# Optimization experiments

Hardware: AMD Instinct MI355X
Metric: run time of the kernel (lower is better)

Reference implementation:

```python
import jax, jax.numpy as jnp
import numpy as np

C = 8; E = 512; HEADS = 8; DH = E // HEADS; M = 256; PINV_ITERS = 6; KW = 33

def layer_norm(x, g, b):
    mu = x.mean(-1, keepdims=True)
    xm = x - mu
    v = (xm * xm).mean(-1, keepdims=True)
    return xm / jnp.sqrt(v + 1e-5) * g + b

def mp_pinv(x, iters=PINV_ITERS):
    # Moore-Penrose pseudoinverse via Newton-Schulz iterations (lucidrains nystrom-attention)
    I = jnp.eye(x.shape[-1], dtype=x.dtype)
    ax = jnp.abs(x)
    z = jnp.swapaxes(x, -1, -2) / (jnp.max(ax.sum(-2)) * jnp.max(ax.sum(-1)))
    for _ in range(iters):
        xz = x @ z
        z = 0.25 * z @ (13. * I - xz @ (15. * I - xz @ (7. * I - xz)))
    return z

def nystrom_attn(x, mask, Wqkv, Wout, bout, conv_w):
    b, n0, d = x.shape
    pad = (-n0) % M  # left-pad so seq divisible by num_landmarks
    x = jnp.pad(x, ((0, 0), (pad, 0), (0, 0)))
    mask = jnp.pad(mask, ((0, 0), (pad, 0)))
    n = n0 + pad
    qkv = (x @ Wqkv).reshape(b, n, 3, HEADS, DH).transpose(2, 0, 3, 1, 4)
    q, k, v = qkv[0], qkv[1], qkv[2]  # [b,h,n,dh]
    mf = mask[:, None, :, None].astype(x.dtype)
    q = q * mf * (DH ** -0.5); k = k * mf; v = v * mf
    l = n // M
    mls = mask.reshape(b, 1, M, l).sum(-1).astype(x.dtype)  # valid count per landmark segment
    div = mls[..., None] + 1e-8
    ql = q.reshape(b, HEADS, M, l, DH).sum(3) / div
    kl = k.reshape(b, HEADS, M, l, DH).sum(3) / div
    mland = mls > 0  # [b,1,M]
    neg = -jnp.finfo(x.dtype).max / 2
    sim1 = jnp.where(mask[:, None, :, None] & mland[..., None, :], jnp.einsum('bhid,bhjd->bhij', q, kl), neg)
    sim2 = jnp.where(mland[..., :, None] & mland[..., None, :], jnp.einsum('bhid,bhjd->bhij', ql, kl), neg)
    sim3 = jnp.where(mland[..., :, None] & mask[:, None, None, :], jnp.einsum('bhid,bhjd->bhij', ql, k), neg)
    a1 = jax.nn.softmax(sim1, -1); a2 = jax.nn.softmax(sim2, -1); a3 = jax.nn.softmax(sim3, -1)
    out = (a1 @ mp_pinv(a2)) @ (a3 @ v)
    # residual depthwise conv over sequence dim (residual=True in NystromAttention)
    out = out + jax.lax.conv_general_dilated(v, conv_w, (1, 1), ((KW // 2, KW // 2), (0, 0)),
                                             dimension_numbers=('NCHW', 'OIHW', 'NCHW'),
                                             feature_group_count=HEADS)
    out = out.transpose(0, 2, 1, 3).reshape(b, n, d) @ Wout + bout
    return out[:, pad:]

def _forward(h, W1, b1, cls_token, pmt_token, ln1_g, ln1_b, Wqkv1, Wout1, bout1, conv1,
             ln0_g, ln0_b, Wqkv0, Wout0, bout0, conv0, lnf_g, lnf_b, W3, b3):
    N = h.shape[0]
    h1 = jax.nn.relu(h @ W1 + b1)  # _fc1
    seq = jnp.concatenate([cls_token, pmt_token, h1], 0)[None]  # [1, 1+C+N, E]
    y = nystrom_attn(layer_norm(seq, ln1_g, ln1_b), jnp.ones((1, seq.shape[1]), bool),
                     Wqkv1, Wout1, bout1, conv1)
    x = seq + y  # layer1 (TransLayer_custom)
    pmt = x[:, 1:1 + C, :]   # new pmt tokens [1,C,E]
    toks = x[:, 1 + C:, :]   # [1,N,E]
    assn = jax.nn.softmax(jnp.einsum('bnd,bcd->bnc', toks, pmt), -1)
    idx = jnp.argmax(assn[0], -1)  # [N] cluster assignment
    # cluster dispatch: per-cluster [pmt_i; tokens-of-cluster-i] run of shared layer0, via masking
    xs = jnp.concatenate([pmt[0][:, None, :], jnp.broadcast_to(toks[0], (C, N, E))], 1)  # [C,1+N,E]
    masks = jnp.concatenate([jnp.ones((C, 1), bool), idx[None, :] == jnp.arange(C)[:, None]], 1)
    def trans0(xi, mi):
        xi = xi[None]
        return (xi + nystrom_attn(layer_norm(xi, ln0_g, ln0_b), mi[None], Wqkv0, Wout0, bout0, conv0))[0]
    out = jax.vmap(trans0)(xs, masks)  # [C,1+N,E]
    h_un = out[:, 1:, :][idx, jnp.arange(N)]  # each token from its own cluster's run
    order = jnp.argsort(idx)  # stable: groups tokens by cluster, preserving order (concat order)
    h_global = h_un[order]; idx_new = idx[order]
    hcat = jnp.concatenate([x[0, 0][None], h_global], 0)  # [1+N, E]
    hn = layer_norm(hcat, lnf_g, lnf_b)
    sums = jax.ops.segment_sum(hcat[1:], idx_new, num_segments=C)
    counts = jax.ops.segment_sum(jnp.ones((N,), h.dtype), idx_new, num_segments=C)
    merge = sums / jnp.maximum(counts, 1.)[:, None]  # CTM merge token per cluster
    ptc = jnp.linalg.norm(pmt[0] @ pmt[0].T - jnp.eye(C, dtype=h.dtype))
    tok_out = jnp.concatenate([hn[0][None], merge], 0).mean(0)
    logit = tok_out @ W3 + b3
    return logit, ptc

def setup_inputs() -> dict:
    key = jax.random.key(0)
    ks = jax.random.split(key, 16)
    N, IN_DIM, NC = 4096, 1024, 2
    s = 0.02
    q, _ = jnp.linalg.qr(jax.random.normal(ks[15], (E, C)))  # orthonormal pmt init
    return {
        'h': jax.random.normal(ks[0], (N, IN_DIM)),
        'W1': jax.random.normal(ks[1], (IN_DIM, E)) * s, 'b1': jnp.zeros((E,)),
        'cls_token': jax.random.normal(ks[2], (1, E)),
        'pmt_token': q.T,
        'ln1_g': jnp.ones((E,)), 'ln1_b': jnp.zeros((E,)),
        'Wqkv1': jax.random.normal(ks[3], (E, 3 * E)) * s,
        'Wout1': jax.random.normal(ks[4], (E, E)) * s, 'bout1': jnp.zeros((E,)),
        'conv1': jax.random.normal(ks[5], (HEADS, 1, KW, 1)) * s,
        'ln0_g': jnp.ones((E,)), 'ln0_b': jnp.zeros((E,)),
        'Wqkv0': jax.random.normal(ks[6], (E, 3 * E)) * s,
        'Wout0': jax.random.normal(ks[7], (E, E)) * s, 'bout0': jnp.zeros((E,)),
        'conv0': jax.random.normal(ks[8], (HEADS, 1, KW, 1)) * s,
        'lnf_g': jnp.ones((E,)), 'lnf_b': jnp.zeros((E,)),
        'W3': jax.random.normal(ks[9], (E, NC)) * s, 'b3': jnp.zeros((NC,)),
    }

def reference(h, W1, b1, cls_token, pmt_token, ln1_g, ln1_b, Wqkv1, Wout1, bout1, conv1,
              ln0_g, ln0_b, Wqkv0, Wout0, bout0, conv0, lnf_g, lnf_b, W3, b3):
    logit, ptc = _forward(h, W1, b1, cls_token, pmt_token, ln1_g, ln1_b, Wqkv1, Wout1, bout1, conv1,
                          ln0_g, ln0_b, Wqkv0, Wout0, bout0, conv0, lnf_g, lnf_b, W3, b3)
    return (logit[None], jax.nn.softmax(logit)[None], ptc)
```

## Files before the change

### kernel.cpp

```cpp
#include <hip/hip_runtime.h>

#define NEGV (-1.70141173e38f)

constexpr int E    = 512;
constexpr int NTOK = 4096;
constexpr int NPAD = 4352;
constexpr int PAD1 = 247;
constexpr int NSEQ = 4105;
constexpr int NG   = 5120;
constexpr int NTP  = 4104;

typedef __attribute__((ext_vector_type(8))) short short8;
typedef __attribute__((ext_vector_type(4))) float float4v;

__device__ inline float bf2f(ushort u){ return __uint_as_float(((unsigned)u)<<16); }
__device__ inline ushort f2bf(float f){
  unsigned u = __float_as_uint(f);
  unsigned r = (u + 0x7FFFu + ((u>>16)&1u)) >> 16;
  return (ushort)r;
}
__device__ inline uint4 packu4(const ushort* u) {
  uint4 w;
  w.x = (unsigned)u[0] | ((unsigned)u[1] << 16);
  w.y = (unsigned)u[2] | ((unsigned)u[3] << 16);
  w.z = (unsigned)u[4] | ((unsigned)u[5] << 16);
  w.w = (unsigned)u[6] | ((unsigned)u[7] << 16);
  return w;
}

template<int BT, bool BOUNDS>
__global__ __launch_bounds__(256) void k_mm(
    const ushort* __restrict__ A, const ushort* __restrict__ B,
    const float* __restrict__ bias, const float* __restrict__ resid,
    float* __restrict__ Cf, ushort* __restrict__ Cb,
    int M, int N, int K, int ksplit, int ldC,
    long sA, long sB, long sC,
    const int* __restrict__ colsel, const int* __restrict__ rowsel,
    int zmodA, int zmodB, const int* __restrict__ krange, int kshift,
    float alpha, float bdiag, int flags)
{
  const int z = blockIdx.z;
  const int batch = z / ksplit, ks = z - batch * ksplit;
  const int kslice = K / ksplit;
  int kbeg = ks * kslice, kend = kbeg + kslice;
  if (krange) { int ki = batch >> kshift; kbeg = krange[2*ki]; kend = krange[2*ki+1]; }
  long aoff;
  if (colsel) { int s = colsel[blockIdx.x]; if (s < 0) s = 0; aoff = (long)(s*8 + batch) * sA; }
  else aoff = (long)(zmodA ? (batch & (zmodA-1)) : batch) * sA;
  long boff;
  if (rowsel) { int s = rowsel[blockIdx.y]; if (s < 0) s = 0; boff = (long)(s*8 + batch) * sB; }
  else boff = (long)(zmodB ? (batch & (zmodB-1)) : batch) * sB;
  A += aoff; B += boff;
  const long coff = (long)z * sC;

  __shared__ __align__(16) ushort Al[4][128][8];
  __shared__ __align__(16) ushort Bl[4][128][8];

  const int tid  = threadIdx.x;
  const int lane = tid & 63, wid = tid >> 6;
  const int wr = wid >> 1, wc = wid & 1;
  const int l4 = lane >> 4, l15 = lane & 15;
  const int row0 = blockIdx.y * 128, col0 = blockIdx.x * 128;

  float4v acc[4][4];
#pragma unroll
  for (int i = 0; i < 4; ++i)
#pragma unroll
    for (int j = 0; j < 4; ++j) acc[i][j] = (float4v){0.f,0.f,0.f,0.f};

  for (int k0 = kbeg; k0 < kend; k0 += 32) {
    __syncthreads();
#pragma unroll
    for (int e = 0; e < 2; ++e) {
      int id = tid * 2 + e; int m = id >> 2, kb = id & 3;
      uint4 v = make_uint4(0u,0u,0u,0u);
      int gr = row0 + m;
      if (!BOUNDS || gr < M)
        v = *reinterpret_cast<const uint4*>(A + (long)gr * K + k0 + kb * 8);
      *reinterpret_cast<uint4*>(&Al[kb][m][0]) = v;
    }
    if (BT) {
#pragma unroll
      for (int e = 0; e < 2; ++e) {
        int id = tid * 2 + e; int n = id >> 2, kb = id & 3;
        uint4 v = make_uint4(0u,0u,0u,0u);
        int gc = col0 + n;
        if (!BOUNDS || gc < N)
          v = *reinterpret_cast<const uint4*>(B + (long)gc * K + k0 + kb * 8);
        *reinterpret_cast<uint4*>(&Bl[kb][n][0]) = v;
      }
    } else {
      int n = tid & 127, gc = col0 + n;
      bool inb = (!BOUNDS || gc < N);
#pragma unroll
      for (int e = 0; e < 2; ++e) {
        int kb = (tid >> 7) * 2 + e;
        ushort u[8];
#pragma unroll
        for (int j = 0; j < 8; ++j) {
          int gk = k0 + kb * 8 + j;
          ushort val = inb ? B[(long)gk * N + gc] : (ushort)0;
          if (flags & 4) {
            float f = bdiag * (gk == gc ? 1.f : 0.f) - bf2f(val);
            val = f2bf(f);
          }
          u[j] = val;
        }
        *reinterpret_cast<uint4*>(&Bl[kb][n][0]) = packu4(u);
      }
    }
    __syncthreads();
    short8 af[4], bg[4];
#pragma unroll
    for (int mi = 0; mi < 4; ++mi)
      af[mi] = *reinterpret_cast<const short8*>(&Al[l4][wr*64 + mi*16 + l15][0]);
#pragma unroll
    for (int ni = 0; ni < 4; ++ni)
      bg[ni] = *reinterpret_cast<const short8*>(&Bl[l4][wc*64 + ni*16 + l15][0]);
#pragma unroll
    for (int mi = 0; mi < 4; ++mi)
#pragma unroll
      for (int ni = 0; ni < 4; ++ni)
        acc[mi][ni] = __builtin_amdgcn_mfma_f32_16x16x32_bf16(af[mi], bg[ni], acc[mi][ni], 0, 0, 0);
  }
#pragma unroll
  for (int mi = 0; mi < 4; ++mi)
#pragma unroll
    for (int ni = 0; ni < 4; ++ni)
#pragma unroll
      for (int r = 0; r < 4; ++r) {
        int row = row0 + wr*64 + mi*16 + l4*4 + r;
        int col = col0 + wc*64 + ni*16 + l15;
        if (BOUNDS && (row >= M || col >= N)) continue;
        float v = alpha * acc[mi][ni][r];
        if (flags & 1) v += bias[col];
        if (flags & 2) v = fmaxf(v, 0.f);
        if (flags & 8) v += resid[(long)row * ldC + col];
        long off = coff + (long)row * ldC + col;
        if (flags & 16) Cb[off] = f2bf(v); else Cf[off] = v;
      }
}

static void mm(hipStream_t st, const void* A, const void* B, const float* bias, const float* resid,
               float* Cf, ushort* Cb, int M, int N, int K, int nb, int ksplit, int ldC,
               long sA, long sB, long sC,
               const int* colsel, const int* rowsel, int zmodA, int zmodB,
               const int* krange, int kshift,
               float alpha, float bdiag, int flags, bool bt, bool bounds)
{
  dim3 g((N + 127) / 128, (M + 127) / 128, nb * ksplit), b(256);
  const ushort* a = (const ushort*)A; const ushort* bb = (const ushort*)B;
  if (bt) {
    if (bounds) k_mm<1, true ><<<g, b, 0, st>>>(a, bb, bias, resid, Cf, Cb, M, N, K, ksplit, ldC, sA, sB, sC, colsel, rowsel, zmodA, zmodB, krange, kshift, alpha, bdiag, flags);
    else        k_mm<1, false><<<g, b, 0, st>>>(a, bb, bias, resid, Cf, Cb, M, N, K, ksplit, ldC, sA, sB, sC, colsel, rowsel, zmodA, zmodB, krange, kshift, alpha, bdiag, flags);
  } else {
    if (bounds) k_mm<0, true ><<<g, b, 0, st>>>(a, bb, bias, resid, Cf, Cb, M, N, K, ksplit, ldC, sA, sB, sC, colsel, rowsel, zmodA, zmodB, krange, kshift, alpha, bdiag, flags);
    else        k_mm<0, false><<<g, b, 0, st>>>(a, bb, bias, resid, Cf, Cb, M, N, K, ksplit, ldC, sA, sB, sC, colsel, rowsel, zmodA, zmodB, krange, kshift, alpha, bdiag, flags);
  }
}

__global__ __launch_bounds__(256, 1) void k_pinv(
    const ushort* __restrict__ X,
    ushort* __restrict__ ZA, ushort* __restrict__ ZAt,
    ushort* __restrict__ ZB, ushort* __restrict__ ZBt,
    ushort* __restrict__ Y,  ushort* __restrict__ Yt,
    ushort* __restrict__ T1, ushort* __restrict__ T1t,
    ushort* __restrict__ T2, ushort* __restrict__ T2t,
    float* __restrict__ sc, int nb, int* __restrict__ bars)
{
  __shared__ __align__(16) ushort SH[8448];
  ushort* AlF = SH;
  ushort* BlF = SH + 4096;
  const int tid = threadIdx.x;
  const int nblk = gridDim.x;
  int bi = 0;

  auto BAR = [&]() {
    __syncthreads();
    if (tid == 0) {
      __threadfence();
      atomicAdd(&bars[bi], 1);
      while (atomicAdd(&bars[bi], 0) < nblk) __builtin_amdgcn_s_sleep(2);
    }
    ++bi;
    __syncthreads();
    __threadfence();
  };

  {
    int ncl = nb >> 3;
    if ((int)blockIdx.x < ncl) {
      float* red = (float*)SH;
      int cl = blockIdx.x;
      float cmax = 0.f;
      for (int h = 0; h < 8; ++h) {
        const ushort* mat = X + (long)(cl * 8 + h) * 65536;
        float cs = 0.f;
        for (int i = 0; i < 256; ++i) cs += bf2f(mat[i * 256 + tid]);
        cmax = fmaxf(cmax, cs);
      }
      red[tid] = cmax; __syncthreads();
      for (int o = 128; o > 0; o >>= 1) { if (tid < o) red[tid] = fmaxf(red[tid], red[tid+o]); __syncthreads(); }
      if (tid == 0) sc[cl] = 1.f / red[0];
    }
    BAR();
  }

  const int ntile = nb * 4;

  {
    ushort (*lds2)[264] = (ushort(*)[264])SH;
    for (int tile = blockIdx.x; tile < ntile; tile += nblk) {
      int bt = tile >> 2, q = tile & 3;
      int row0 = (q >> 1) * 128, col0 = (q & 1) * 128;
      float scale = sc[bt >> 3];
      const ushort* Xb = X + (long)bt * 65536;
      ushort* Z0  = ZA  + (long)bt * 65536;
      ushort* Z0t = ZAt + (long)bt * 65536;
#pragma unroll
      for (int e = 0; e < 8; ++e) {
        int id = tid + e * 256;
        int r = id >> 4, ch = (id & 15) * 8;
        const ushort* src = Xb + (long)(row0 + r) * 256 + col0 + ch;
        ushort u[8];
#pragma unroll
        for (int j = 0; j < 8; ++j) u[j] = f2bf(bf2f(src[j]) * scale);
        *reinterpret_cast<uint4*>(Z0t + (long)(row0 + r) * 256 + col0 + ch) = packu4(u);
      }
      for (int s = 0; s < 4; ++s) {
        __syncthreads();
#pragma unroll
        for (int e = 0; e < 2; ++e) {
          int id = tid * 2 + e;
          int sr = id >> 4, ch = (id & 15) * 8;
          *reinterpret_cast<uint4*>(&lds2[sr][ch]) =
            *reinterpret_cast<const uint4*>(Xb + (long)(col0 + s * 32 + sr) * 256 + row0 + ch);
        }
        __syncthreads();
#pragma unroll
        for (int e = 0; e < 2; ++e) {
          int id = tid * 2 + e;
          int orow = id >> 2, oseg = (id & 3) * 8;
          ushort u[8];
#pragma unroll
          for (int j = 0; j < 8; ++j) u[j] = f2bf(bf2f(lds2[oseg + j][orow]) * scale);
          *reinterpret_cast<uint4*>(Z0 + (long)(row0 + orow) * 256 + col0 + s * 32 + oseg) = packu4(u);
        }
      }
      __syncthreads();
    }
    BAR();
  }

  const int lane = tid & 63, wid = tid >> 6;
  const int wr = wid >> 1, wc = wid & 1;
  const int l4 = lane >> 4, l15 = lane & 15;

  auto GEMM = [&](const ushort* A, const ushort* Bt, ushort* C, ushort* Ct,
                  float alpha, float bdiag, bool diag) {
    for (int tile = blockIdx.x; tile < ntile; tile += nblk) {
      int bt = tile >> 2, q = tile & 3;
      int row0 = (q >> 1) * 128, col0 = (q & 1) * 128;
      const ushort* Ab = A + (long)bt * 65536;
      const ushort* Bb = Bt + (long)bt * 65536;
      float4v acc[4][4];
#pragma unroll
      for (int i = 0; i < 4; ++i)
#pragma unroll
        for (int j = 0; j < 4; ++j) acc[i][j] = (float4v){0.f,0.f,0.f,0.f};
      for (int k0 = 0; k0 < 256; k0 += 32) {
        __syncthreads();
#pragma unroll
        for (int e = 0; e < 2; ++e) {
          int id = tid * 2 + e; int m = id >> 2, kb = id & 3;
          *reinterpret_cast<uint4*>(AlF + kb * 1024 + m * 8) =
            *reinterpret_cast<const uint4*>(Ab + (long)(row0 + m) * 256 + k0 + kb * 8);
        }
#pragma unroll
        for (int e = 0; e < 2; ++e) {
          int id = tid * 2 + e; int n = id >> 2, kb = id & 3;
          uint4 v = *reinterpret_cast<const uint4*>(Bb + (long)(col0 + n) * 256 + k0 + kb * 8);
          if (diag) {
            const ushort* up = reinterpret_cast<const ushort*>(&v);
            ushort u2[8];
#pragma unroll
            for (int j = 0; j < 8; ++j) {
              int gk = k0 + kb * 8 + j;
              u2[j] = f2bf(bdiag * (gk == (col0 + n) ? 1.f : 0.f) - bf2f(up[j]));
            }
            v = packu4(u2);
          }
          *reinterpret_cast<uint4*>(BlF + kb * 1024 + n * 8) = v;
        }
        __syncthreads();
        short8 af[4], bg[4];
#pragma unroll
        for (int mi = 0; mi < 4; ++mi)
          af[mi] = *reinterpret_cast<const short8*>(AlF + l4 * 1024 + (wr * 64 + mi * 16 + l15) * 8);
#pragma unroll
        for (int ni = 0; ni < 4; ++ni)
          bg[ni] = *reinterpret_cast<const short8*>(BlF + l4 * 1024 + (wc * 64 + ni * 16 + l15) * 8);
#pragma unroll
        for (int mi = 0; mi < 4; ++mi)
#pragma unroll
          for (int ni = 0; ni < 4; ++ni)
            acc[mi][ni] = __builtin_amdgcn_mfma_f32_16x16x32_bf16(af[mi], bg[ni], acc[mi][ni], 0, 0, 0);
      }
      long cb = (long)bt * 65536;
#pragma unroll
      for (int mi = 0; mi < 4; ++mi)
#pragma unroll
        for (int ni = 0; ni < 4; ++ni)
#pragma unroll
          for (int r = 0; r < 4; ++r) {
            int row = row0 + wr * 64 + mi * 16 + l4 * 4 + r;
            int col = col0 + wc * 64 + ni * 16 + l15;
            ushort val = f2bf(alpha * acc[mi][ni][r]);
            C[cb + (long)row * 256 + col] = val;
            Ct[cb + (long)col * 256 + row] = val;
          }
      __syncthreads();
    }
  };

  for (int it = 0; it < 6; ++it) {
    ushort* Zc  = (it & 1) ? ZB  : ZA;
    ushort* Zct = (it & 1) ? ZBt : ZAt;
    ushort* Zn  = (it & 1) ? ZA  : ZB;
    ushort* Znt = (it & 1) ? ZAt : ZBt;
    GEMM(X,  Zct, Y,  Yt,  1.f,    0.f, false); BAR();
    GEMM(Y,  Yt,  T1, T1t, 1.f,    7.f, true);  BAR();
    GEMM(Y,  T1t, T2, T2t, 1.f,   15.f, true);  BAR();
    GEMM(Zc, T2t, Zn, Znt, 0.25f, 13.f, true);
    if (it < 5) BAR();
  }
}

__global__ void k_prep0(const float* __restrict__ cls, const float* __restrict__ pmt, float* __restrict__ seq) {
  int i = blockIdx.x * 256 + threadIdx.x;
  if (i < 512) seq[i] = cls[i];
  else if (i < 4608) seq[i] = pmt[i - 512];
}
__global__ void k_cvt(const float* __restrict__ s, ushort* __restrict__ d, long n) {
  long i = (long)blockIdx.x * 256 + threadIdx.x;
  if (i < n) d[i] = f2bf(s[i]);
}
__global__ void k_tcvt_all(const float* __restrict__ W1, const float* __restrict__ Wq1,
                           const float* __restrict__ Wq0, const float* __restrict__ Wo1,
                           const float* __restrict__ Wo0,
                           ushort* __restrict__ W1t, ushort* __restrict__ Wq1t,
                           ushort* __restrict__ Wq0t, ushort* __restrict__ Wo1t,
                           ushort* __restrict__ Wo0t) {
  const float* W; ushort* Wt; int K, N;
  switch (blockIdx.z) {
    case 0:  W = W1;  Wt = W1t;  K = 1024; N = 512;  break;
    case 1:  W = Wq1; Wt = Wq1t; K = 512;  N = 1536; break;
    case 2:  W = Wq0; Wt = Wq0t; K = 512;  N = 1536; break;
    case 3:  W = Wo1; Wt = Wo1t; K = 512;  N = 512;  break;
    default: W = Wo0; Wt = Wo0t; K = 512;  N = 512;  break;
  }
  int nb_ = blockIdx.x * 32, kb = blockIdx.y * 32;
  if (nb_ >= N || kb >= K) return;
  __shared__ float tile[32][33];
  int tx = threadIdx.x, ty = threadIdx.y;
  for (int r = ty; r < 32; r += 8) tile[r][tx] = W[(long)(kb + r) * N + nb_ + tx];
  __syncthreads();
  for (int r = ty; r < 32; r += 8) Wt[(long)(nb_ + r) * K + kb + tx] = f2bf(tile[tx][r]);
}

__device__ __forceinline__ void ln_row(const float* __restrict__ xr, const float* __restrict__ g,
                                       const float* __restrict__ b, ushort* __restrict__ yr,
                                       float* red, int t) {
  float v0 = xr[t], v1 = xr[t + 256];
  red[t] = v0 + v1; __syncthreads();
  for (int o = 128; o > 0; o >>= 1) { if (t < o) red[t] += red[t + o]; __syncthreads(); }
  float mu = red[0] * (1.f / E); __syncthreads();
  float d0 = v0 - mu, d1 = v1 - mu;
  red[t] = d0 * d0 + d1 * d1; __syncthreads();
  for (int o = 128; o > 0; o >>= 1) { if (t < o) red[t] += red[t + o]; __syncthreads(); }
  float inv = 1.f / sqrtf(red[0] * (1.f / E) + 1e-5f);
  yr[t]       = f2bf(d0 * inv * g[t]       + b[t]);
  yr[t + 256] = f2bf(d1 * inv * g[t + 256] + b[t + 256]);
}

__global__ __launch_bounds__(256) void k_lnB(const float* __restrict__ x, const float* __restrict__ g,
                                             const float* __restrict__ b, ushort* __restrict__ y) {
  int row = blockIdx.x, t = threadIdx.x;
  ushort* yr = y + (long)row * E;
  if (row < PAD1) { yr[t] = 0; yr[t + 256] = 0; return; }
  __shared__ float red[256];
  ln_row(x + (long)(row - PAD1) * E, g, b, yr, red, t);
}
__global__ __launch_bounds__(256) void k_lnC(const float* __restrict__ seq, const float* __restrict__ g,
                                             const float* __restrict__ b, ushort* __restrict__ y) {
  int row = blockIdx.x, t = threadIdx.x;
  const float* xr = (row < 8) ? (seq + 512 + (long)row * E) : (seq + 9 * 512 + (long)(row - 8) * E);
  __shared__ float red[256];
  ln_row(xr, g, b, y + (long)row * E, red, t);
}

__global__ void k_buildQKVB(const float* __restrict__ qkv, ushort* __restrict__ Qb,
                            ushort* __restrict__ Kb, ushort* __restrict__ Vt) {
  int h = blockIdx.y, p0 = blockIdx.x * 64;
  int tx = threadIdx.x & 63, tg = threadIdx.x >> 6;
  __shared__ float tile[64][65];
  for (int r = tg; r < 64; r += 4) {
    long src = (long)(p0 + r) * 1536 + h * 64 + tx;
    long o = ((long)h * NPAD + p0 + r) * 64 + tx;
    Qb[o] = f2bf(qkv[src]);
    Kb[o] = f2bf(qkv[src + 512]);
    tile[r][tx] = qkv[src + 1024];
  }
  __syncthreads();
  for (int d = tg; d < 64; d += 4) Vt[((long)h * 64 + d) * NPAD + p0 + tx] = f2bf(tile[tx][d]);
}
__global__ void k_gatherQKV(const float* __restrict__ qkvall, const int* __restrict__ gtok,
                            ushort* __restrict__ Qg, ushort* __restrict__ Kg, ushort* __restrict__ Vgt) {
  int h = blockIdx.y, p0 = blockIdx.x * 64;
  int tx = threadIdx.x & 63, tg = threadIdx.x >> 6;
  __shared__ float tile[64][65];
  for (int r = tg; r < 64; r += 4) {
    int tk = gtok[p0 + r];
    int srcrow = tk >= 0 ? 8 + tk : (tk <= -2 ? (-2 - tk) : -1);
    float q = 0.f, k = 0.f, v = 0.f;
    if (srcrow >= 0) {
      long s = (long)srcrow * 1536 + h * 64 + tx;
      q = qkvall[s]; k = qkvall[s + 512]; v = qkvall[s + 1024];
    }
    long o = ((long)h * NG + p0 + r) * 64 + tx;
    Qg[o] = f2bf(q); Kg[o] = f2bf(k);
    tile[r][tx] = v;
  }
  __syncthreads();
  for (int d = tg; d < 64; d += 4) Vgt[((long)h * 64 + d) * NG + p0 + tx] = f2bf(tile[tx][d]);
}

__global__ void k_qlkl_B(const float* __restrict__ qkv, ushort* __restrict__ ql, ushort* __restrict__ kl,
                         float* __restrict__ mlandB) {
  int i = blockIdx.x, h = blockIdx.y, d = threadIdx.x;
  float sq = 0.f, sk = 0.f; int cnt = 0;
  for (int j = 0; j < 17; ++j) {
    int p = i * 17 + j;
    if (p >= PAD1) {
      sq += qkv[(long)p * 1536 + h * 64 + d];
      sk += qkv[(long)p * 1536 + 512 + h * 64 + d];
      cnt++;
    }
  }
  float dv = (float)cnt + 1e-8f;
  ql[((long)h * 256 + i) * 64 + d] = f2bf(sq * 0.125f / dv);
  kl[((long)h * 256 + i) * 64 + d] = f2bf(sk / dv);
  if (h == 0 && d == 0) mlandB[i] = cnt > 0 ? 1.f : 0.f;
}

__global__ void k_qlkl_C(const float* __restrict__ qkvall, const int* __restrict__ idx,
                         ushort* __restrict__ qlc, ushort* __restrict__ klc,
                         float* __restrict__ mland_c) {
  int i = blockIdx.x, bt = blockIdx.y;
  int c = bt >> 3, h = bt & 7, d = threadIdx.x;
  float sq = 0.f, sk = 0.f; int cnt = 0;
  for (int j = 0; j < 17; ++j) {
    int p = i * 17 + j;
    int srcrow = -1;
    if (p == 255) srcrow = c;
    else if (p >= 256 && idx[p - 256] == c) srcrow = 8 + (p - 256);
    if (srcrow >= 0) {
      const float* src = qkvall + (long)srcrow * 1536 + h * 64;
      sq += src[d]; sk += src[512 + d];
      cnt++;
    }
  }
  float dv = (float)cnt + 1e-8f;
  qlc[((long)bt * 256 + i) * 64 + d] = f2bf(sq * 0.125f / dv);
  klc[((long)bt * 256 + i) * 64 + d] = f2bf(sk / dv);
  if (h == 0 && d == 0) mland_c[c * 256 + i] = cnt > 0 ? 1.f : 0.f;
}

__global__ __launch_bounds__(256) void k_a2soft(const float* __restrict__ S2, const float* __restrict__ mland,
                                                ushort* __restrict__ X) {
  int i = blockIdx.x, bt = blockIdx.y, j = threadIdx.x;
  int cl = bt >> 3;
  const float* Sr = S2 + ((long)bt * 256 + i) * 256;
  __shared__ float red[256];
  float landi = mland[cl * 256 + i];
  float out;
  if (landi > 0.f) {
    bool valid = mland[cl * 256 + j] > 0.f;
// ... 182 lines not shown
  }
  if (t == 0) {
    int s = 0;
    for (int c = 0; c < 8; ++c) {
      segs[c] = s;
      base[c] = s + 1;
      int tt2 = 1 + tot[c];
      krange[2 * c] = s;
      krange[2 * c + 1] = s + ((tt2 + 31) & ~31);
      s += (tt2 + 127) & ~127;
    }
    segs[8] = s;
    for (int c = 0; c <= 8; ++c) segb[c] = segs[c];
  }
  __syncthreads();
  for (int g = t; g < NG; g += 256) { gtok[g] = -1; gclu[g] = -1; }
  __syncthreads();
  if (t < 8) { gtok[segs[t]] = -2 - t; gclu[segs[t]] = t; }
  for (int b = t; b < NG / 128; b += 256) {
    int cl = -1;
    for (int c = 0; c < 8; ++c) if (b * 128 >= segs[c] && b * 128 < segs[c + 1]) cl = c;
    blkclu[b] = cl;
  }
  for (int b = 0; b < 16; ++b) {
    int c = myc[b];
    int rankw = 0;
    for (int cc = 0; cc < 8; ++cc) {
      unsigned long long m = __ballot(c == cc);
      if (c == cc) rankw = __popcll(m & ltmask);
      if (lane == 0) wcnt[w][cc] = __popcll(m);
    }
    __syncthreads();
    int off = base[c] + rankw;
    for (int w2 = 0; w2 < w; ++w2) off += wcnt[w2][c];
    int n = b * 256 + t;
    gtok[off] = n; gclu[off] = c; gpos[n] = off;
    __syncthreads();
    if (t < 8) base[t] += wcnt[0][t] + wcnt[1][t] + wcnt[2][t] + wcnt[3][t];
    __syncthreads();
  }
}

__global__ void k_outC(const float* __restrict__ OUTg, const int* __restrict__ gpos,
                       const int* __restrict__ idx, const float* __restrict__ qkvall,
                       const float* __restrict__ w, ushort* __restrict__ lnb) {
  int n = blockIdx.x, t = threadIdx.x;
  int h = t >> 6;
  int c = idx[n];
  float acc = OUTg[(long)gpos[n] * 512 + t];
  for (int tt = 0; tt < 33; ++tt) {
    int m = n + tt - 16;
    float vv = 0.f;
    if (m == -1) vv = qkvall[(long)c * 1536 + 1024 + t];
    else if (m >= 0 && m < NTOK && idx[m] == c) vv = qkvall[(long)(8 + m) * 1536 + 1024 + t];
    acc += vv * w[h * 33 + tt];
  }
  lnb[(long)n * E + t] = f2bf(acc);
}

__global__ void k_seg_part(const float* __restrict__ hun, const int* __restrict__ idx,
                           float* __restrict__ part, float* __restrict__ pcnt) {
  int c = blockIdx.x, sl = blockIdx.y, d = threadIdx.x;
  float s = 0.f; int cnt = 0;
  for (int n = sl * 256; n < sl * 256 + 256; ++n) {
    if (idx[n] == c) { s += hun[(long)n * E + d]; if (d == 0) cnt++; }
  }
  part[(long)(c * 16 + sl) * E + d] = s;
  if (d == 0) pcnt[c * 16 + sl] = (float)cnt;
}

__global__ void k_final(const float* __restrict__ x0, const float* __restrict__ g, const float* __restrict__ b,
                        const float* __restrict__ part, const float* __restrict__ pcnt,
                        const float* __restrict__ ptc, const float* __restrict__ W3, const float* __restrict__ b3,
                        float* __restrict__ out) {
  int t = threadIdx.x;
  __shared__ float red[512];
  float xv = x0[t];
  red[t] = xv; __syncthreads();
  for (int o = 256; o > 0; o >>= 1) { if (t < o) red[t] += red[t + o]; __syncthreads(); }
  float mu = red[0] * (1.f / 512.f); __syncthreads();
  float d0 = xv - mu;
  red[t] = d0 * d0; __syncthreads();
  for (int o = 256; o > 0; o >>= 1) { if (t < o) red[t] += red[t + o]; __syncthreads(); }
  float inv = 1.f / sqrtf(red[0] * (1.f / 512.f) + 1e-5f);
  __syncthreads();
  float acc = d0 * inv * g[t] + b[t];
  for (int c = 0; c < 8; ++c) {
    float s = 0.f, cnt = 0.f;
    for (int sl = 0; sl < 16; ++sl) { s += part[(long)(c * 16 + sl) * E + t]; cnt += pcnt[c * 16 + sl]; }
    acc += s / fmaxf(cnt, 1.f);
  }
  float tk = acc * (1.f / 9.f);
  red[t] = tk * W3[t * 2 + 0]; __syncthreads();
  for (int o = 256; o > 0; o >>= 1) { if (t < o) red[t] += red[t + o]; __syncthreads(); }
  float l0 = red[0] + b3[0]; __syncthreads();
  red[t] = tk * W3[t * 2 + 1]; __syncthreads();
  for (int o = 256; o > 0; o >>= 1) { if (t < o) red[t] += red[t + o]; __syncthreads(); }
  float l1 = red[0] + b3[1];
  if (t == 0) {
    out[0] = l0; out[1] = l1;
    float mx = fmaxf(l0, l1);
    float e0 = expf(l0 - mx), e1 = expf(l1 - mx), s = e0 + e1;
    out[2] = e0 / s; out[3] = e1 / s;
    out[4] = *ptc;
  }
}

extern "C" void kernel_launch(void* const* d_in, const int* in_sizes, int n_in,
                              void* d_out, int out_size, void* d_ws, size_t ws_size,
                              hipStream_t stream) {
  const float* h_in  = (const float*)d_in[0];
  const float* W1    = (const float*)d_in[1];
  const float* b1    = (const float*)d_in[2];
  const float* cls   = (const float*)d_in[3];
  const float* pmt_t = (const float*)d_in[4];
  const float* ln1_g = (const float*)d_in[5];
  const float* ln1_b = (const float*)d_in[6];
  const float* Wqkv1 = (const float*)d_in[7];
  const float* Wout1 = (const float*)d_in[8];
  const float* bout1 = (const float*)d_in[9];
  const float* conv1 = (const float*)d_in[10];
  const float* ln0_g = (const float*)d_in[11];
  const float* ln0_b = (const float*)d_in[12];
  const float* Wqkv0 = (const float*)d_in[13];
  const float* Wout0 = (const float*)d_in[14];
  const float* bout0 = (const float*)d_in[15];
  const float* conv0 = (const float*)d_in[16];
  const float* lnf_g = (const float*)d_in[17];
  const float* lnf_b = (const float*)d_in[18];
  const float* W3    = (const float*)d_in[19];
  const float* b3    = (const float*)d_in[20];

  char* base = (char*)d_ws;
  size_t off = 0;
  auto alloc = [&](size_t b) -> void* {
    off = (off + 255) & ~(size_t)255;
    void* p = base + off; off += b; return p;
  };
  float*  SEQ    = (float*) alloc((size_t)NSEQ * E * 4);
  float*  QKV    = (float*) alloc((size_t)NPAD * 1536 * 4);
  ushort* W1t    = (ushort*)alloc((size_t)512 * 1024 * 2);
  ushort* Wq1t   = (ushort*)alloc((size_t)1536 * 512 * 2);
  ushort* Wq0t   = (ushort*)alloc((size_t)1536 * 512 * 2);
  ushort* Wo1t   = (ushort*)alloc((size_t)512 * 512 * 2);
  ushort* Wo0t   = (ushort*)alloc((size_t)512 * 512 * 2);
  ushort* LNb    = (ushort*)alloc((size_t)NPAD * E * 2);
  ushort* QbU    = (ushort*)alloc((size_t)8 * NG * 64 * 2);
  ushort* KbU    = (ushort*)alloc((size_t)8 * NG * 64 * 2);
  ushort* VtU    = (ushort*)alloc((size_t)8 * NG * 64 * 2);
  char*   U1     = (char*)  alloc((size_t)8 * 256 * NG * 4);
  char*   U2     = (char*)  alloc((size_t)8 * 256 * NG * 2);
  ushort* PXb    = (ushort*)alloc((size_t)64 * 65536 * 2);
  ushort* PZa    = (ushort*)alloc((size_t)64 * 65536 * 2);
  ushort* PZat   = (ushort*)alloc((size_t)64 * 65536 * 2);
  ushort* qlbB   = (ushort*)alloc((size_t)8 * 16384 * 2);
  ushort* klbB   = (ushort*)alloc((size_t)8 * 16384 * 2);
  ushort* qlcb   = (ushort*)alloc((size_t)64 * 16384 * 2);
  ushort* klcb   = (ushort*)alloc((size_t)64 * 16384 * 2);
  float*  avsl   = (float*) alloc((size_t)8 * 8 * 16384 * 4);
  ushort* avb    = (ushort*)alloc((size_t)64 * 16384 * 2);
  ushort* Wcb    = (ushort*)alloc((size_t)64 * 16384 * 2);
  float*  PREOUT = (float*) alloc((size_t)NPAD * E * 4);
  float*  mlandB = (float*) alloc(256 * 4);
  float*  mlandC = (float*) alloc(8 * 256 * 4);
  int*    idx    = (int*)   alloc(NTOK * 4);
  int*    gtok   = (int*)   alloc(NG * 4);
  int*    gclu   = (int*)   alloc(NG * 4);
  int*    gpos   = (int*)   alloc(NTOK * 4);
  int*    segb   = (int*)   alloc(9 * 4);
  int*    krange = (int*)   alloc(16 * 4);
  int*    blkclu = (int*)   alloc((NG / 128) * 4);
  float*  ptc    = (float*) alloc(256);
  float*  sc     = (float*) alloc(256);
  int*    bars   = (int*)   alloc(64 * 4);
  float*  part   = (float*) alloc((size_t)8 * 16 * 512 * 4);
  float*  pcnt   = (float*) alloc(8 * 16 * 4);

  ushort* hb   = (ushort*)U1;
  float*  Sbuf = (float*)U1;
  ushort* Yp   = (ushort*)U1;
  ushort* Ytp  = (ushort*)(U1 + 1L * 8388608);
  ushort* T1p  = (ushort*)(U1 + 2L * 8388608);
  ushort* T1tp = (ushort*)(U1 + 3L * 8388608);
  ushort* T2p  = (ushort*)(U1 + 4L * 8388608);
  float*  OUTg = (float*)U1;
  ushort* Pbuf = (ushort*)U2;
  ushort* ZBp  = (ushort*)U2;
  ushort* ZBtp = (ushort*)U2 + 4194304;
  ushort* T2tp = (ushort*)avsl;

  hipMemsetAsync(bars, 0, 64 * sizeof(int), stream);

  k_tcvt_all<<<dim3(48, 32, 5), dim3(32, 8), 0, stream>>>(W1, Wqkv1, Wqkv0, Wout1, Wout0,
                                                          W1t, Wq1t, Wq0t, Wo1t, Wo0t);
  k_prep0<<<dim3(18), dim3(256), 0, stream>>>(cls, pmt_t, SEQ);
  k_cvt<<<dim3(16384), dim3(256), 0, stream>>>(h_in, hb, (long)4096 * 1024);
  mm(stream, hb, W1t, b1, nullptr, SEQ + 9 * 512, nullptr, 4096, 512, 1024, 1, 1, 512,
     0, 0, 0, nullptr, nullptr, 0, 0, nullptr, 0, 1.f, 0.f, 1 | 2, true, false);

  k_lnB<<<dim3(NPAD), dim3(256), 0, stream>>>(SEQ, ln1_g, ln1_b, LNb);
  mm(stream, LNb, Wq1t, nullptr, nullptr, QKV, nullptr, NPAD, 1536, 512, 1, 1, 1536,
     0, 0, 0, nullptr, nullptr, 0, 0, nullptr, 0, 1.f, 0.f, 0, true, false);
  k_buildQKVB<<<dim3(NPAD / 64, 8), dim3(256), 0, stream>>>(QKV, QbU, KbU, VtU);
  k_qlkl_B<<<dim3(256, 8), dim3(64), 0, stream>>>(QKV, qlbB, klbB, mlandB);
  mm(stream, qlbB, klbB, nullptr, nullptr, Sbuf, nullptr, 256, 256, 64, 8, 1, 256,
     16384, 16384, 65536, nullptr, nullptr, 0, 0, nullptr, 0, 1.f, 0.f, 0, true, false);
  k_a2soft<<<dim3(256, 8), dim3(256), 0, stream>>>(Sbuf, mlandB, PXb);
  k_pinv<<<dim3(256), dim3(256), 0, stream>>>(PXb, PZa, PZat, ZBp, ZBtp, Yp, Ytp, T1p, T1tp, T2p, T2tp,
                                              sc, 8, bars);
  mm(stream, qlbB, KbU, nullptr, nullptr, Sbuf, nullptr, 256, NPAD, 64, 8, 1, NPAD,
     16384, (long)NPAD * 64, (long)256 * NPAD, nullptr, nullptr, 0, 0, nullptr, 0, 1.f, 0.f, 0, true, false);
  k_smaxB_av<<<dim3(256, 8), dim3(256), 0, stream>>>(Sbuf, Pbuf, mlandB);
  mm(stream, Pbuf, VtU, nullptr, nullptr, avsl, nullptr, 256, 64, NPAD, 8, 8, 64,
     (long)256 * NPAD, (long)64 * NPAD, 16384, nullptr, nullptr, 0, 0, nullptr, 0, 1.f, 0.f, 0, true, true);
  k_avredB<<<dim3(256, 8), dim3(64), 0, stream>>>(avsl, avb, 8);
  mm(stream, PZa, avb, nullptr, nullptr, nullptr, Wcb, 256, 64, 256, 8, 1, 64,
     65536, 16384, 16384, nullptr, nullptr, 0, 0, nullptr, 0, 1.f, 0.f, 16, false, true);
  mm(stream, QbU + PAD1 * 64, klbB, nullptr, nullptr, Sbuf, nullptr, NSEQ, 256, 64, 8, 1, 256,
     (long)NPAD * 64, 16384, (long)NSEQ * 256, nullptr, nullptr, 0, 0, nullptr, 0, 0.125f, 0.f, 0, true, true);
  k_smax256<0><<<dim3(NSEQ, 8), dim3(256), 0, stream>>>(Sbuf, Pbuf, mlandB, nullptr, nullptr, NSEQ);
  mm(stream, Pbuf, Wcb, nullptr, nullptr, PREOUT + (long)PAD1 * 512, nullptr, NSEQ, 64, 256, 8, 1, 512,
     (long)NSEQ * 256, 16384, 64, nullptr, nullptr, 0, 0, nullptr, 0, 1.f, 0.f, 0, false, true);
  k_conv_B<<<dim3(NSEQ), dim3(512), 0, stream>>>(QKV, conv1, PREOUT, LNb);
  mm(stream, LNb, Wo1t, bout1, SEQ, SEQ, nullptr, NSEQ, 512, 512, 1, 1, 512,
     0, 0, 0, nullptr, nullptr, 0, 0, nullptr, 0, 1.f, 0.f, 1 | 8, true, true);

  k_idxptc<<<dim3(NTOK + 1), dim3(64), 0, stream>>>(SEQ, idx, ptc);
  k_gprep<<<dim3(1), dim3(256), 0, stream>>>(idx, gtok, gclu, gpos, segb, krange, blkclu);
  k_lnC<<<dim3(NTP), dim3(256), 0, stream>>>(SEQ, ln0_g, ln0_b, LNb);
  mm(stream, LNb, Wq0t, nullptr, nullptr, QKV, nullptr, NTP, 1536, 512, 1, 1, 1536,
     0, 0, 0, nullptr, nullptr, 0, 0, nullptr, 0, 1.f, 0.f, 0, true, true);
  k_qlkl_C<<<dim3(256, 64), dim3(64), 0, stream>>>(QKV, idx, qlcb, klcb, mlandC);
  k_gatherQKV<<<dim3(NG / 64, 8), dim3(256), 0, stream>>>(QKV, gtok, QbU, KbU, VtU);
  mm(stream, qlcb, klcb, nullptr, nullptr, Sbuf, nullptr, 256, 256, 64, 64, 1, 256,
     16384, 16384, 65536, nullptr, nullptr, 0, 0, nullptr, 0, 1.f, 0.f, 0, true, false);
  k_a2soft<<<dim3(256, 64), dim3(256), 0, stream>>>(Sbuf, mlandC, PXb);
  k_pinv<<<dim3(256), dim3(256), 0, stream>>>(PXb, PZa, PZat, ZBp, ZBtp, Yp, Ytp, T1p, T1tp, T2p, T2tp,
                                              sc, 64, bars + 32);
  mm(stream, qlcb, KbU, nullptr, nullptr, Sbuf, nullptr, 256, NG, 64, 8, 1, NG,
     16384, (long)NG * 64, (long)256 * NG, blkclu, nullptr, 0, 0, nullptr, 0, 1.f, 0.f, 0, true, false);
  k_smaxseg<<<dim3(256, 64), dim3(256), 0, stream>>>(Sbuf, Pbuf, mlandC, gclu, segb);
  mm(stream, Pbuf, VtU, nullptr, nullptr, nullptr, avb, 256, 64, NG, 64, 1, 64,
     (long)256 * NG, (long)64 * NG, 16384, nullptr, nullptr, 8, 8, krange, 3, 1.f, 0.f, 16, true, true);
  mm(stream, PZa, avb, nullptr, nullptr, nullptr, Wcb, 256, 64, 256, 64, 1, 64,
     65536, 16384, 16384, nullptr, nullptr, 0, 0, nullptr, 0, 1.f, 0.f, 16, false, true);
  mm(stream, QbU, klcb, nullptr, nullptr, Sbuf, nullptr, NG, 256, 64, 8, 1, 256,
     (long)NG * 64, 16384, (long)NG * 256, nullptr, blkclu, 0, 0, nullptr, 0, 0.125f, 0.f, 0, true, false);
  k_smax256<1><<<dim3(NG, 8), dim3(256), 0, stream>>>(Sbuf, Pbuf, mlandC, gtok, gclu, NG);
  mm(stream, Pbuf, Wcb, nullptr, nullptr, OUTg, nullptr, NG, 64, 256, 8, 1, 512,
     (long)NG * 256, 16384, 64, nullptr, blkclu, 0, 0, nullptr, 0, 1.f, 0.f, 0, false, true);
  k_outC<<<dim3(NTOK), dim3(512), 0, stream>>>(OUTg, gpos, idx, QKV, conv0, LNb);
  mm(stream, LNb, Wo0t, bout0, SEQ + 9 * 512, PREOUT, nullptr, NTOK, 512, 512, 1, 1, 512,
     0, 0, 0, nullptr, nullptr, 0, 0, nullptr, 0, 1.f, 0.f, 1 | 8, true, false);

  k_seg_part<<<dim3(8, 16), dim3(512), 0, stream>>>(PREOUT, idx, part, pcnt);
  k_final<<<dim3(1), dim3(512), 0, stream>>>(SEQ, lnf_g, lnf_b, part, pcnt, ptc, W3, b3,
                                             (float*)d_out);
}
```

Measured before the change: 2.993 ms.

## Restructure pinv persistent kernel: smaller tiles, no transposed copies, more blocks

Rewrites the Newton-Schulz pseudoinverse persistent kernel. It now uses 128x64 output tiles across 512 blocks with two blocks per CU, and computes the column-sum max in parallel with one block per matrix combined via atomicMax. It also drops the duplicate transposed output writes, transposing the B operand through LDS inside the GEMM instead. This removes half the global stores and the extra buffers, and spreads the barrier-separated GEMM phases over more blocks, at the cost of an extra LDS transpose stage and sync per k-step. Tile-to-block assignment is strided so each block's work follows a different ordering.

```diff
diff --git a/kernel.cpp b/kernel.cpp
--- a/kernel.cpp
+++ b/kernel.cpp
@@ -159,20 +159,19 @@
   }
 }
 
-__global__ __launch_bounds__(256, 1) void k_pinv(
+__global__ __launch_bounds__(256, 2) void k_pinv(
     const ushort* __restrict__ X,
-    ushort* __restrict__ ZA, ushort* __restrict__ ZAt,
-    ushort* __restrict__ ZB, ushort* __restrict__ ZBt,
-    ushort* __restrict__ Y,  ushort* __restrict__ Yt,
-    ushort* __restrict__ T1, ushort* __restrict__ T1t,
-    ushort* __restrict__ T2, ushort* __restrict__ T2t,
-    float* __restrict__ sc, int nb, int* __restrict__ bars)
+    ushort* __restrict__ ZA, ushort* __restrict__ ZB,
+    ushort* __restrict__ Y, ushort* __restrict__ T1, ushort* __restrict__ T2,
+    unsigned* __restrict__ scmax, int nb, int* __restrict__ bars)
 {
-  __shared__ __align__(16) ushort SH[8448];
-  ushort* AlF = SH;
-  ushort* BlF = SH + 4096;
+  __shared__ __align__(16) ushort Al[4][128][8];
+  __shared__ __align__(16) ushort TRB[32][68];
+  __shared__ __align__(16) ushort Bl[4][64][12];
+  __shared__ __align__(16) ushort TR[32][136];
+  __shared__ float red[256];
   const int tid = threadIdx.x;
-  const int nblk = gridDim.x;
+  const int b = blockIdx.x, nblk = gridDim.x;
   int bi = 0;
 
   auto BAR = [&]() {
@@ -187,152 +186,133 @@
     __threadfence();
   };
 
+  if (b < nb) {
+    const ushort* mat = X + (long)b * 65536;
+    float cs = 0.f;
+    for (int i = 0; i < 256; ++i) cs += bf2f(mat[i * 256 + tid]);
+    red[tid] = cs; __syncthreads();
+    for (int o = 128; o > 0; o >>= 1) { if (tid < o) red[tid] = fmaxf(red[tid], red[tid + o]); __syncthreads(); }
+    if (tid == 0) atomicMax(&scmax[b >> 3], __float_as_uint(red[0]));
+  }
+  BAR();
+
   {
-    int ncl = nb >> 3;
-    if ((int)blockIdx.x < ncl) {
-      float* red = (float*)SH;
-      int cl = blockIdx.x;
-      float cmax = 0.f;
-      for (int h = 0; h < 8; ++h) {
-        const ushort* mat = X + (long)(cl * 8 + h) * 65536;
-        float cs = 0.f;
-        for (int i = 0; i < 256; ++i) cs += bf2f(mat[i * 256 + tid]);
-        cmax = fmaxf(cmax, cs);
-      }
-      red[tid] = cmax; __syncthreads();
-      for (int o = 128; o > 0; o >>= 1) { if (tid < o) red[tid] = fmaxf(red[tid], red[tid+o]); __syncthreads(); }
-      if (tid == 0) sc[cl] = 1.f / red[0];
-    }
-    BAR();
-  }
-
-  const int ntile = nb * 4;
-
-  {
-    ushort (*lds2)[264] = (ushort(*)[264])SH;
-    for (int tile = blockIdx.x; tile < ntile; tile += nblk) {
-      int bt = tile >> 2, q = tile & 3;
+    int nxt = (nb * 4) >> 3;
+    for (int i = b >> 3; i < nxt; i += 64) {
+      int t = (b & 7) * nxt + i;
+      int bt = t >> 2, q = t & 3;
       int row0 = (q >> 1) * 128, col0 = (q & 1) * 128;
-      float scale = sc[bt >> 3];
       const ushort* Xb = X + (long)bt * 65536;
-      ushort* Z0  = ZA  + (long)bt * 65536;
-      ushort* Z0t = ZAt + (long)bt * 65536;
-#pragma unroll
-      for (int e = 0; e < 8; ++e) {
-        int id = tid + e * 256;
-        int r = id >> 4, ch = (id & 15) * 8;
-        const ushort* src = Xb + (long)(row0 + r) * 256 + col0 + ch;
-        ushort u[8];
-#pragma unroll
-        for (int j = 0; j < 8; ++j) u[j] = f2bf(bf2f(src[j]) * scale);
-        *reinterpret_cast<uint4*>(Z0t + (long)(row0 + r) * 256 + col0 + ch) = packu4(u);
-      }
+      float scale = 1.f / __uint_as_float(scmax[bt >> 3]);
       for (int s = 0; s < 4; ++s) {
         __syncthreads();
 #pragma unroll
         for (int e = 0; e < 2; ++e) {
-          int id = tid * 2 + e;
-          int sr = id >> 4, ch = (id & 15) * 8;
-          *reinterpret_cast<uint4*>(&lds2[sr][ch]) =
+          int id = tid * 2 + e; int sr = id >> 4, ch = (id & 15) * 8;
+          *reinterpret_cast<uint4*>(&TR[sr][ch]) =
             *reinterpret_cast<const uint4*>(Xb + (long)(col0 + s * 32 + sr) * 256 + row0 + ch);
         }
         __syncthreads();
 #pragma unroll
         for (int e = 0; e < 2; ++e) {
-          int id = tid * 2 + e;
-          int orow = id >> 2, oseg = (id & 3) * 8;
+          int id = tid * 2 + e; int orow = id >> 2, oseg = (id & 3) * 8;
           ushort u[8];
 #pragma unroll
-          for (int j = 0; j < 8; ++j) u[j] = f2bf(bf2f(lds2[oseg + j][orow]) * scale);
-          *reinterpret_cast<uint4*>(Z0 + (long)(row0 + orow) * 256 + col0 + s * 32 + oseg) = packu4(u);
+          for (int j = 0; j < 8; ++j) u[j] = f2bf(bf2f(TR[oseg + j][orow]) * scale);
+          *reinterpret_cast<uint4*>(ZA + (long)bt * 65536 + (long)(row0 + orow) * 256 + col0 + s * 32 + oseg) = packu4(u);
         }
       }
       __syncthreads();
     }
-    BAR();
-  }
-
-  const int lane = tid & 63, wid = tid >> 6;
-  const int wr = wid >> 1, wc = wid & 1;
+  }
+  BAR();
+
+  const int lane = tid & 63, w = tid >> 6;
   const int l4 = lane >> 4, l15 = lane & 15;
 
-  auto GEMM = [&](const ushort* A, const ushort* Bt, ushort* C, ushort* Ct,
+  auto GEMM = [&](const ushort* Ag, const ushort* Bg, ushort* Cg,
                   float alpha, float bdiag, bool diag) {
-    for (int tile = blockIdx.x; tile < ntile; tile += nblk) {
-      int bt = tile >> 2, q = tile & 3;
-      int row0 = (q >> 1) * 128, col0 = (q & 1) * 128;
-      const ushort* Ab = A + (long)bt * 65536;
-      const ushort* Bb = Bt + (long)bt * 65536;
-      float4v acc[4][4];
-#pragma unroll
-      for (int i = 0; i < 4; ++i)
-#pragma unroll
-        for (int j = 0; j < 4; ++j) acc[i][j] = (float4v){0.f,0.f,0.f,0.f};
+    const int nx = nb;
+    for (int i = b >> 3; i < nx; i += 64) {
+      const int t = (b & 7) * nx + i;
+      const int bt = t >> 3, q = t & 7;
+      const int row0 = (q >> 2) * 128, col0 = (q & 3) * 64;
+      const ushort* Ab = Ag + (long)bt * 65536;
+      const ushort* Bb = Bg + (long)bt * 65536;
+      float4v acc[2][4];
+#pragma unroll
+      for (int mi = 0; mi < 2; ++mi)
+#pragma unroll
+        for (int ni = 0; ni < 4; ++ni) acc[mi][ni] = (float4v){0.f,0.f,0.f,0.f};
+
       for (int k0 = 0; k0 < 256; k0 += 32) {
         __syncthreads();
+        { int gk = tid >> 3, c8 = (tid & 7) * 8;
+          *reinterpret_cast<uint4*>(&TRB[gk][c8]) =
+            *reinterpret_cast<const uint4*>(Bb + (long)(k0 + gk) * 256 + col0 + c8); }
+        __syncthreads();
 #pragma unroll
         for (int e = 0; e < 2; ++e) {
           int id = tid * 2 + e; int m = id >> 2, kb = id & 3;
-          *reinterpret_cast<uint4*>(AlF + kb * 1024 + m * 8) =
+          *reinterpret_cast<uint4*>(&Al[kb][m][0]) =
             *reinterpret_cast<const uint4*>(Ab + (long)(row0 + m) * 256 + k0 + kb * 8);
         }
-#pragma unroll
-        for (int e = 0; e < 2; ++e) {
-          int id = tid * 2 + e; int n = id >> 2, kb = id & 3;
-          uint4 v = *reinterpret_cast<const uint4*>(Bb + (long)(col0 + n) * 256 + k0 + kb * 8);
-          if (diag) {
-            const ushort* up = reinterpret_cast<const ushort*>(&v);
-            ushort u2[8];
-#pragma unroll
-            for (int j = 0; j < 8; ++j) {
-              int gk = k0 + kb * 8 + j;
-              u2[j] = f2bf(bdiag * (gk == (col0 + n) ? 1.f : 0.f) - bf2f(up[j]));
+        { int kb = tid >> 6, n = tid & 63;
+          ushort u[8];
+#pragma unroll
+          for (int j = 0; j < 8; ++j) {
+            ushort val = TRB[kb * 8 + j][n];
+            if (diag) {
+              int gkA = k0 + kb * 8 + j, gcA = col0 + n;
+              val = f2bf(bdiag * (gkA == gcA ? 1.f : 0.f) - bf2f(val));
             }
-            v = packu4(u2);
+            u[j] = val;
           }
-          *reinterpret_cast<uint4*>(BlF + kb * 1024 + n * 8) = v;
+          unsigned long long d0 = (unsigned long long)u[0] | ((unsigned long long)u[1] << 16) |
+                                  ((unsigned long long)u[2] << 32) | ((unsigned long long)u[3] << 48);
+          unsigned long long d1 = (unsigned long long)u[4] | ((unsigned long long)u[5] << 16) |
+                                  ((unsigned long long)u[6] << 32) | ((unsigned long long)u[7] << 48);
+          unsigned long long* dst = reinterpret_cast<unsigned long long*>(&Bl[kb][n][0]);
+          dst[0] = d0; dst[1] = d1;
         }
         __syncthreads();
-        short8 af[4], bg[4];
-#pragma unroll
-        for (int mi = 0; mi < 4; ++mi)
-          af[mi] = *reinterpret_cast<const short8*>(AlF + l4 * 1024 + (wr * 64 + mi * 16 + l15) * 8);
+        union { short8 v; unsigned long long d[2]; } bgv[4];
+#pragma unroll
+        for (int ni = 0; ni < 4; ++ni) {
+          const unsigned long long* sp = reinterpret_cast<const unsigned long long*>(&Bl[l4][ni * 16 + l15][0]);
+          bgv[ni].d[0] = sp[0]; bgv[ni].d[1] = sp[1];
+        }
+#pragma unroll
+        for (int mi = 0; mi < 2; ++mi) {
+          short8 af = *reinterpret_cast<const short8*>(&Al[l4][w * 32 + mi * 16 + l15][0]);
+#pragma unroll
+          for (int ni = 0; ni < 4; ++ni)
+            acc[mi][ni] = __builtin_amdgcn_mfma_f32_16x16x32_bf16(af, bgv[ni].v, acc[mi][ni], 0, 0, 0);
+        }
+      }
+      const long cb = (long)bt * 65536;
+#pragma unroll
+      for (int mi = 0; mi < 2; ++mi)
 #pragma unroll
         for (int ni = 0; ni < 4; ++ni)
-          bg[ni] = *reinterpret_cast<const short8*>(BlF + l4 * 1024 + (wc * 64 + ni * 16 + l15) * 8);
-#pragma unroll
-        for (int mi = 0; mi < 4; ++mi)
-#pragma unroll
-          for (int ni = 0; ni < 4; ++ni)
-            acc[mi][ni] = __builtin_amdgcn_mfma_f32_16x16x32_bf16(af[mi], bg[ni], acc[mi][ni], 0, 0, 0);
-      }
-      long cb = (long)bt * 65536;
-#pragma unroll
-      for (int mi = 0; mi < 4; ++mi)
-#pragma unroll
-        for (int ni = 0; ni < 4; ++ni)
 #pragma unroll
           for (int r = 0; r < 4; ++r) {
-            int row = row0 + wr * 64 + mi * 16 + l4 * 4 + r;
-            int col = col0 + wc * 64 + ni * 16 + l15;
-            ushort val = f2bf(alpha * acc[mi][ni][r]);
-            C[cb + (long)row * 256 + col] = val;
-            Ct[cb + (long)col * 256 + row] = val;
+            int row = row0 + w * 32 + mi * 16 + l4 * 4 + r;
+            int col = col0 + ni * 16 + l15;
+            Cg[cb + (long)row * 256 + col] = f2bf(alpha * acc[mi][ni][r]);
           }
       __syncthreads();
     }
   };
 
+  ushort* Zc = ZA; ushort* Zn = ZB;
   for (int it = 0; it < 6; ++it) {
-    ushort* Zc  = (it & 1) ? ZB  : ZA;
-    ushort* Zct = (it & 1) ? ZBt : ZAt;
-    ushort* Zn  = (it & 1) ? ZA  : ZB;
-    ushort* Znt = (it & 1) ? ZAt : ZBt;
-    GEMM(X,  Zct, Y,  Yt,  1.f,    0.f, false); BAR();
-    GEMM(Y,  Yt,  T1, T1t, 1.f,    7.f, true);  BAR();
-    GEMM(Y,  T1t, T2, T2t, 1.f,   15.f, true);  BAR();
-    GEMM(Zc, T2t, Zn, Znt, 0.25f, 13.f, true);
+    GEMM(X,  Zc, Y,  1.f,   0.f,  false); BAR();
+    GEMM(Y,  Y,  T1, 1.f,   7.f,  true);  BAR();
+    GEMM(Y,  T1, T2, 1.f,   15.f, true);  BAR();
+    GEMM(Zc, T2, Zn, 0.25f, 13.f, true);
     if (it < 5) BAR();
+    ushort* tmp = Zc; Zc = Zn; Zn = tmp;
   }
 }
 
@@ -821,7 +801,6 @@
   char*   U2     = (char*)  alloc((size_t)8 * 256 * NG * 2);
   ushort* PXb    = (ushort*)alloc((size_t)64 * 65536 * 2);
   ushort* PZa    = (ushort*)alloc((size_t)64 * 65536 * 2);
-  ushort* PZat   = (ushort*)alloc((size_t)64 * 65536 * 2);
   ushort* qlbB   = (ushort*)alloc((size_t)8 * 16384 * 2);
   ushort* klbB   = (ushort*)alloc((size_t)8 * 16384 * 2);
   ushort* qlcb   = (ushort*)alloc((size_t)64 * 16384 * 2);
@@ -840,25 +819,21 @@
   int*    krange = (int*)   alloc(16 * 4);
   int*    blkclu = (int*)   alloc((NG / 128) * 4);
   float*  ptc    = (float*) alloc(256);
-  float*  sc     = (float*) alloc(256);
-  int*    bars   = (int*)   alloc(64 * 4);
+  int*    bars   = (int*)   alloc(80 * 4);
   float*  part   = (float*) alloc((size_t)8 * 16 * 512 * 4);
   float*  pcnt   = (float*) alloc(8 * 16 * 4);
+  unsigned* scmax = (unsigned*)(bars + 64);
 
   ushort* hb   = (ushort*)U1;
   float*  Sbuf = (float*)U1;
   ushort* Yp   = (ushort*)U1;
-  ushort* Ytp  = (ushort*)(U1 + 1L * 8388608);
-  ushort* T1p  = (ushort*)(U1 + 2L * 8388608);
-  ushort* T1tp = (ushort*)(U1 + 3L * 8388608);
-  ushort* T2p  = (ushort*)(U1 + 4L * 8388608);
+  ushort* T1p  = (ushort*)(U1 + 1L * 8388608);
+  ushort* T2p  = (ushort*)(U1 + 2L * 8388608);
+  ushort* ZBp  = (ushort*)(U1 + 3L * 8388608);
   float*  OUTg = (float*)U1;
   ushort* Pbuf = (ushort*)U2;
-  ushort* ZBp  = (ushort*)U2;
-  ushort* ZBtp = (ushort*)U2 + 4194304;
-  ushort* T2tp = (ushort*)avsl;
-
-  hipMemsetAsync(bars, 0, 64 * sizeof(int), stream);
+
+  hipMemsetAsync(bars, 0, 80 * sizeof(int), stream);
 
   k_tcvt_all<<<dim3(48, 32, 5), dim3(32, 8), 0, stream>>>(W1, Wqkv1, Wqkv0, Wout1, Wout0,
                                                           W1t, Wq1t, Wq0t, Wo1t, Wo0t);
@@ -875,8 +850,7 @@
   mm(stream, qlbB, klbB, nullptr, nullptr, Sbuf, nullptr, 256, 256, 64, 8, 1, 256,
      16384, 16384, 65536, nullptr, nullptr, 0, 0, nullptr, 0, 1.f, 0.f, 0, true, false);
   k_a2soft<<<dim3(256, 8), dim3(256), 0, stream>>>(Sbuf, mlandB, PXb);
-  k_pinv<<<dim3(256), dim3(256), 0, stream>>>(PXb, PZa, PZat, ZBp, ZBtp, Yp, Ytp, T1p, T1tp, T2p, T2tp,
-                                              sc, 8, bars);
+  k_pinv<<<dim3(512), dim3(256), 0, stream>>>(PXb, PZa, ZBp, Yp, T1p, T2p, scmax, 8, bars);
   mm(stream, qlbB, KbU, nullptr, nullptr, Sbuf, nullptr, 256, NPAD, 64, 8, 1, NPAD,
      16384, (long)NPAD * 64, (long)256 * NPAD, nullptr, nullptr, 0, 0, nullptr, 0, 1.f, 0.f, 0, true, false);
   k_smaxB_av<<<dim3(256, 8), dim3(256), 0, stream>>>(Sbuf, Pbuf, mlandB);
@@ -904,8 +878,7 @@
   mm(stream, qlcb, klcb, nullptr, nullptr, Sbuf, nullptr, 256, 256, 64, 64, 1, 256,
      16384, 16384, 65536, nullptr, nullptr, 0, 0, nullptr, 0, 1.f, 0.f, 0, true, false);
   k_a2soft<<<dim3(256, 64), dim3(256), 0, stream>>>(Sbuf, mlandC, PXb);
-  k_pinv<<<dim3(256), dim3(256), 0, stream>>>(PXb, PZa, PZat, ZBp, ZBtp, Yp, Ytp, T1p, T1tp, T2p, T2tp,
-                                              sc, 64, bars + 32);
+  k_pinv<<<dim3(512), dim3(256), 0, stream>>>(PXb, PZa, ZBp, Yp, T1p, T2p, scmax + 8, 64, bars + 32);
   mm(stream, qlcb, KbU, nullptr, nullptr, Sbuf, nullptr, 256, NG, 64, 8, 1, NG,
      16384, (long)NG * 64, (long)256 * NG, blkclu, nullptr, 0, 0, nullptr, 0, 1.f, 0.f, 0, true, false);
   k_smaxseg<<<dim3(256, 64), dim3(256), 0, stream>>>(Sbuf, Pbuf, mlandC, gclu, segb);
```

Measured after the change: 4.566 ms (median of 4 runs). +52.6%, slower.
